# Kernel tuning notes

Hardware: AMD Instinct MI355X
Metric: run time of the kernel (lower is better)

Reference implementation:

```python
import jax, jax.numpy as jnp
import numpy as np
from jax import lax

B, L, D_MODEL = 8, 2048, 512
D_STATE, D_CONV, EXPAND = 16, 4, 2
D_INNER = EXPAND * D_MODEL          # 1024
DT_RANK = (D_MODEL + 15) // 16      # 32


def setup_inputs() -> dict:
    key = jax.random.key(0)
    ks = jax.random.split(key, 12)
    g = lambda k, shape, s=0.02: jax.random.normal(k, shape, jnp.float32) * s
    inp = {
        "p_history": jax.random.normal(ks[0], (B, L, D_MODEL), jnp.float32),
        "W_in":   g(ks[1], (2 * D_INNER, D_MODEL)),
        "conv_w": g(ks[2], (D_INNER, D_CONV), 0.1),
        "conv_b": jnp.zeros((D_INNER,), jnp.float32),
        "W_x":    g(ks[3], (DT_RANK + 2 * D_STATE, D_INNER)),
        "W_dt":   g(ks[4], (D_INNER, DT_RANK), 0.1),
        "b_dt":   g(ks[5], (D_INNER,), 0.5),
        "A_log":  jnp.log(jnp.broadcast_to(jnp.arange(1, D_STATE + 1, dtype=jnp.float32), (D_INNER, D_STATE))),
        "D":      jnp.ones((D_INNER,), jnp.float32),
        "W_out":  g(ks[6], (D_MODEL, D_INNER)),
        "ln_g":   jnp.ones((D_MODEL,), jnp.float32),
        "ln_b":   jnp.zeros((D_MODEL,), jnp.float32),
        "W_head": g(ks[7], (D_MODEL, D_MODEL)),
        "b_head": jnp.zeros((D_MODEL,), jnp.float32),
    }
    return inp


def _mamba_forward(p_history, W_in, conv_w, conv_b, W_x, W_dt, b_dt, A_log, D, W_out):
    # input projection -> x (ssm branch) and z (gate branch), each [B, L, d_inner]
    xz = jnp.einsum("bld,ed->ble", p_history, W_in)
    x, z = jnp.split(xz, 2, axis=-1)

    # depthwise causal conv over L: [B, d_inner, L]
    xc = x.swapaxes(1, 2)
    xc = lax.conv_general_dilated(
        xc, conv_w[:, None, :], window_strides=(1,),
        padding=[(D_CONV - 1, 0)], feature_group_count=D_INNER,
        dimension_numbers=("NCH", "OIH", "NCH"))
    xc = xc + conv_b[None, :, None]
    x = jax.nn.silu(xc.swapaxes(1, 2))  # [B, L, d_inner]

    # input-dependent dt, B, C
    x_dbl = jnp.einsum("blf,ef->ble", x, W_x)
    dt, Bm, Cm = jnp.split(x_dbl, [DT_RANK, DT_RANK + D_STATE], axis=-1)
    dt = jax.nn.softplus(jnp.einsum("blr,er->ble", dt, W_dt) + b_dt)  # [B, L, d_inner]

    A = -jnp.exp(A_log)  # [d_inner, d_state]

    def step(h, inp):
        dt_t, B_t, C_t, x_t = inp                   # [B,d_inner],[B,d_state],[B,d_state],[B,d_inner]
        dA = jnp.exp(dt_t[..., None] * A)           # [B, d_inner, d_state]
        h = dA * h + dt_t[..., None] * B_t[:, None, :] * x_t[..., None]
        y = jnp.einsum("bds,bs->bd", h, C_t)
        return h, y

    h0 = jnp.zeros((B, D_INNER, D_STATE), x.dtype)
    _, ys = lax.scan(step, h0, (dt.swapaxes(0, 1), Bm.swapaxes(0, 1),
                                Cm.swapaxes(0, 1), x.swapaxes(0, 1)))
    y = ys.swapaxes(0, 1) + x * D                   # skip connection
    y = y * jax.nn.silu(z)
    return jnp.einsum("ble,de->bld", y, W_out)      # [B, L, d_model]


def reference(p_history, W_in, conv_w, conv_b, W_x, W_dt, b_dt, A_log, D, W_out,
              ln_g, ln_b, W_head, b_head):
    out = _mamba_forward(p_history, W_in, conv_w, conv_b, W_x, W_dt, b_dt, A_log, D, W_out)
    mu = out.mean(-1, keepdims=True)
    var = ((out - mu) ** 2).mean(-1, keepdims=True)
    xn = (out - mu) * lax.rsqrt(var + 1e-5) * ln_g + ln_b
    return jnp.einsum("bd,ed->be", xn[:, -1, :], W_head) + b_head  # [B, d_model]
```

## Files before the change

### kernel.cpp

```cpp
#include <hip/hip_runtime.h>


#define NB 8
#define SEQ 2048
#define DM 512
#define DI 1024
#define DS 16
#define DR 32
#define NTOK (NB*SEQ)
#define NCH 64
#define CHL (SEQ/NCH)

typedef __attribute__((ext_vector_type(8))) short short8;
typedef __attribute__((ext_vector_type(4))) float f32x4;

__device__ __forceinline__ float b2f(unsigned short u){
  union { unsigned int i; float f; } v; v.i = ((unsigned int)u) << 16; return v.f;
}
__device__ __forceinline__ unsigned short f2b(float f){
  union { unsigned int i; float f; } v; v.f = f;
  unsigned int r = (v.i + 0x7FFFu + ((v.i >> 16) & 1u)) >> 16;
  return (unsigned short)r;
}
__device__ __forceinline__ float silu_(float x){ return x / (1.f + __expf(-x)); }
__device__ __forceinline__ float softplus_(float x){
  return fmaxf(x, 0.f) + __logf(1.f + __expf(-fabsf(x)));
}

typedef __attribute__((address_space(1))) const unsigned int g_u32;
typedef __attribute__((address_space(3))) unsigned int l_u32;
__device__ __forceinline__ void gl16(const void* g, void* l){
  __builtin_amdgcn_global_load_lds((g_u32*)g, (l_u32*)l, 16, 0, 0);
}

__global__ __launch_bounds__(256) void k_cvt(const float* __restrict__ src,
                                             unsigned short* __restrict__ dst, int n4){
  int i = blockIdx.x * 256 + threadIdx.x;
  if (i < n4){
    float4 v = reinterpret_cast<const float4*>(src)[i];
    ushort4 o;
    o.x = f2b(v.x); o.y = f2b(v.y); o.z = f2b(v.z); o.w = f2b(v.w);
    reinterpret_cast<ushort4*>(dst)[i] = o;
  }
}

__global__ __launch_bounds__(256) void k_cvt3(const float* __restrict__ s0, const float* __restrict__ s1,
                                              const float* __restrict__ s2,
                                              unsigned short* __restrict__ d0_, unsigned short* __restrict__ d1_,
                                              unsigned short* __restrict__ d2_){
  int i = blockIdx.x * 256 + threadIdx.x;
  const float* s; unsigned short* d; int j;
  if (i < 131072){ s = s0; d = d0_; j = i; }
  else if (i < 147456){ s = s1; d = d1_; j = i - 131072; }
  else { s = s2; d = d2_; j = i - 147456; }
  float4 v = reinterpret_cast<const float4*>(s)[j];
  ushort4 o; o.x = f2b(v.x); o.y = f2b(v.y); o.z = f2b(v.z); o.w = f2b(v.w);
  reinterpret_cast<ushort4*>(d)[j] = o;
}

__global__ __launch_bounds__(256) void k_gemm_x(const unsigned short* __restrict__ Ag,
                                                const unsigned short* __restrict__ Bg,
                                                unsigned short* __restrict__ xraw){
  __shared__ __align__(16) unsigned short smA[128*64];
  __shared__ __align__(16) unsigned short smB[128*64];
  int tid  = threadIdx.x;
  int lane = tid & 63, wv = tid >> 6;
  int wr = wv >> 1, wc = wv & 1;
  int m0 = blockIdx.x * 128;
  int n0 = blockIdx.y * 128;
  int r16 = lane & 15, kg = lane >> 4;
  f32x4 acc[4][4];
  #pragma unroll
  for (int i = 0; i < 4; ++i)
    #pragma unroll
    for (int j = 0; j < 4; ++j) acc[i][j] = (f32x4){0.f,0.f,0.f,0.f};

  for (int kt = 0; kt < 8; ++kt){
    int k0 = kt * 64;
    #pragma unroll
    for (int r = 0; r < 4; ++r){
      int seg = r * 4 + wv;
      int row = seg * 8 + (lane >> 3);
      int c16 = (lane & 7) ^ (row & 7);
      gl16(Ag + (size_t)(m0 + row) * DM + k0 + c16 * 8, smA + seg * 512);
      gl16(Bg + (size_t)(n0 + row) * DM + k0 + c16 * 8, smB + seg * 512);
    }
    asm volatile("s_waitcnt vmcnt(0)" ::: "memory");
    __syncthreads();
    #pragma unroll
    for (int kk = 0; kk < 2; ++kk){
      short8 af[4], bf[4];
      #pragma unroll
      for (int mt = 0; mt < 4; ++mt){
        int row = wr * 64 + mt * 16 + r16;
        int c16 = ((kk << 2) | kg) ^ (row & 7);
        af[mt] = *reinterpret_cast<const short8*>(smA + row * 64 + c16 * 8);
      }
      #pragma unroll
      for (int nt = 0; nt < 4; ++nt){
        int row = wc * 64 + nt * 16 + r16;
        int c16 = ((kk << 2) | kg) ^ (row & 7);
        bf[nt] = *reinterpret_cast<const short8*>(smB + row * 64 + c16 * 8);
      }
      #pragma unroll
      for (int mt = 0; mt < 4; ++mt)
        #pragma unroll
        for (int nt = 0; nt < 4; ++nt)
          acc[mt][nt] = __builtin_amdgcn_mfma_f32_16x16x32_bf16(af[mt], bf[nt], acc[mt][nt], 0, 0, 0);
    }
    __syncthreads();
  }
  #pragma unroll
  for (int mt = 0; mt < 4; ++mt){
    int rbase = m0 + wr * 64 + mt * 16 + kg * 4;
    #pragma unroll
    for (int nt = 0; nt < 4; ++nt){
      int col = n0 + wc * 64 + nt * 16 + r16;
      #pragma unroll
      for (int r = 0; r < 4; ++r)
        xraw[(size_t)(rbase + r) * DI + col] = f2b(acc[mt][nt][r]);
    }
  }
}

__global__ __launch_bounds__(256) void k_conv(const unsigned short* __restrict__ xraw,
                                              const float* __restrict__ cw,
                                              const float* __restrict__ cb,
                                              unsigned short* __restrict__ xc){
  int tid = threadIdx.x;
  int e4  = tid << 2;
  int t0  = blockIdx.x * 16;
  int l0  = t0 & (SEQ - 1);
  float4 cw0 = reinterpret_cast<const float4*>(cw)[e4 + 0];
  float4 cw1 = reinterpret_cast<const float4*>(cw)[e4 + 1];
  float4 cw2 = reinterpret_cast<const float4*>(cw)[e4 + 2];
  float4 cw3 = reinterpret_cast<const float4*>(cw)[e4 + 3];
  float4 cb4 = *reinterpret_cast<const float4*>(cb + e4);
  float4 wm3, wm2, wm1;
  if (l0 == 0){
    wm3 = wm2 = wm1 = (float4){0.f, 0.f, 0.f, 0.f};
  } else {
    ushort4 a = *reinterpret_cast<const ushort4*>(xraw + (size_t)(t0 - 3) * DI + e4);
    ushort4 b = *reinterpret_cast<const ushort4*>(xraw + (size_t)(t0 - 2) * DI + e4);
    ushort4 c = *reinterpret_cast<const ushort4*>(xraw + (size_t)(t0 - 1) * DI + e4);
    wm3 = (float4){b2f(a.x), b2f(a.y), b2f(a.z), b2f(a.w)};
    wm2 = (float4){b2f(b.x), b2f(b.y), b2f(b.z), b2f(b.w)};
    wm1 = (float4){b2f(c.x), b2f(c.y), b2f(c.z), b2f(c.w)};
  }
  #pragma unroll 4
  for (int t = t0; t < t0 + 16; ++t){
    ushort4 xv = *reinterpret_cast<const ushort4*>(xraw + (size_t)t * DI + e4);
    float4 xf = (float4){b2f(xv.x), b2f(xv.y), b2f(xv.z), b2f(xv.w)};
    float a0 = cb4.x + cw0.x*wm3.x + cw0.y*wm2.x + cw0.z*wm1.x + cw0.w*xf.x;
    float a1 = cb4.y + cw1.x*wm3.y + cw1.y*wm2.y + cw1.z*wm1.y + cw1.w*xf.y;
    float a2 = cb4.z + cw2.x*wm3.z + cw2.y*wm2.z + cw2.z*wm1.z + cw2.w*xf.z;
    float a3 = cb4.w + cw3.x*wm3.w + cw3.y*wm2.w + cw3.z*wm1.w + cw3.w*xf.w;
    ushort4 o;
    o.x = f2b(silu_(a0)); o.y = f2b(silu_(a1)); o.z = f2b(silu_(a2)); o.w = f2b(silu_(a3));
    *reinterpret_cast<ushort4*>(xc + (size_t)t * DI + e4) = o;
    wm3 = wm2; wm2 = wm1; wm1 = xf;
  }
}

__global__ __launch_bounds__(256) void k_bfx(const unsigned short* __restrict__ Wxb,
                                             unsigned short* __restrict__ Bfx){
  int i = blockIdx.x * 256 + threadIdx.x;
  int lane = i & 63, nt = (i >> 6) & 3, kk = (i >> 8) & 1, s = i >> 9;
  short8 v = *reinterpret_cast<const short8*>(
      Wxb + (size_t)(nt * 16 + (lane & 15)) * DI + s * 64 + kk * 32 + (lane >> 4) * 8);
  *reinterpret_cast<short8*>(Bfx + (size_t)i * 8) = v;
}

__global__ __launch_bounds__(256) void k_gemm_xdbl(const unsigned short* __restrict__ xc,
                                                   const unsigned short* __restrict__ Bfx,
                                                   float* __restrict__ xpart){
  __shared__ __align__(16) unsigned short smA[64*64];
  int tid  = threadIdx.x;
  int lane = tid & 63, wv = tid >> 6;
  int m0 = blockIdx.x * 64;
  int ks = blockIdx.y;
  int r16 = lane & 15, kg = lane >> 4;
  f32x4 acc[4];
  #pragma unroll
  for (int i = 0; i < 4; ++i) acc[i] = (f32x4){0.f,0.f,0.f,0.f};
  for (int kt = 0; kt < 8; ++kt){
    int k0 = ks * 512 + kt * 64;
    #pragma unroll
    for (int r = 0; r < 2; ++r){
      int seg = r * 4 + wv;
      int row = seg * 8 + (lane >> 3);
      int c16 = (lane & 7) ^ (row & 7);
      gl16(xc + (size_t)(m0 + row) * DI + k0 + c16 * 8, smA + seg * 512);
    }
    asm volatile("s_waitcnt vmcnt(0)" ::: "memory");
    __syncthreads();
    int sglob = ks * 8 + kt;
    #pragma unroll
    for (int kk = 0; kk < 2; ++kk){
      int row = wv * 16 + r16;
      int c16 = ((kk << 2) | kg) ^ (row & 7);
      short8 af = *reinterpret_cast<const short8*>(smA + row * 64 + c16 * 8);
      #pragma unroll
      for (int nt = 0; nt < 4; ++nt){
        short8 bf = *reinterpret_cast<const short8*>(
            Bfx + ((((size_t)sglob * 2 + kk) * 4 + nt) * 64 + lane) * 8);
        acc[nt] = __builtin_amdgcn_mfma_f32_16x16x32_bf16(af, bf, acc[nt], 0, 0, 0);
      }
    }
    __syncthreads();
  }
  float* xp = xpart + (size_t)ks * NTOK * 64;
  int rbase = m0 + wv * 16 + kg * 4;
  #pragma unroll
  for (int nt = 0; nt < 4; ++nt){
    int col = nt * 16 + r16;
    #pragma unroll
    for (int r = 0; r < 4; ++r)
      xp[(size_t)(rbase + r) * 64 + col] = acc[nt][r];
  }
}

__global__ __launch_bounds__(256) void k_xdbl_fin(const float* __restrict__ xp0,
                                                  const float* __restrict__ xp1,
                                                  float* __restrict__ xdbl,
                                                  unsigned short* __restrict__ dtraw){
  int i = blockIdx.x * 256 + threadIdx.x;
  float4 a = reinterpret_cast<const float4*>(xp0)[i];
  float4 b = reinterpret_cast<const float4*>(xp1)[i];
  float4 s = (float4){a.x + b.x, a.y + b.y, a.z + b.z, a.w + b.w};
  reinterpret_cast<float4*>(xdbl)[i] = s;
  int c4 = i & 15;
  if (c4 < 8){
    int row = i >> 4;
    ushort4 o;
    o.x = f2b(s.x); o.y = f2b(s.y); o.z = f2b(s.z); o.w = f2b(s.w);
    *reinterpret_cast<ushort4*>(dtraw + (size_t)row * DR + c4 * 4) = o;
  }
}

__global__ __launch_bounds__(256) void k_dt(const unsigned short* __restrict__ dtraw,
                                            const unsigned short* __restrict__ Wdtb,
                                            const float* __restrict__ bdt,
                                            unsigned short* __restrict__ dtb){
  int lane = threadIdx.x & 63;
  int wv   = threadIdx.x >> 6;
  int m0 = blockIdx.x * 64 + wv * 16;
  int r16 = lane & 15;
  int kg  = lane >> 4;
  short8 a = *reinterpret_cast<const short8*>(dtraw + (size_t)(m0 + r16) * DR + kg * 8);
  #pragma unroll
  for (int nt = 0; nt < 4; ++nt){
    int n0 = blockIdx.y * 64 + nt * 16;
    short8 b = *reinterpret_cast<const short8*>(Wdtb + (size_t)(n0 + r16) * DR + kg * 8);
    f32x4 acc = {0.f, 0.f, 0.f, 0.f};
    acc = __builtin_amdgcn_mfma_f32_16x16x32_bf16(a, b, acc, 0, 0, 0);
    int rbase = m0 + kg * 4;
    int col = n0 + r16;
    float bb = bdt[col];
    #pragma unroll
    for (int r = 0; r < 4; ++r)
      dtb[(size_t)(rbase + r) * DI + col] = f2b(softplus_(acc[r] + bb));
  }
}

__global__ __launch_bounds__(256) void k_zlast(const float* __restrict__ P,
                                               const float* __restrict__ Win,
                                               float* __restrict__ zl){
  __shared__ float sP[DM];
  int b = blockIdx.y, tid = threadIdx.x;
  const float* pr = P + ((size_t)b * SEQ + (SEQ - 1)) * DM;
  if (tid < 128) reinterpret_cast<float4*>(sP)[tid] = reinterpret_cast<const float4*>(pr)[tid];
  __syncthreads();
  int e  = blockIdx.x * 32 + (tid >> 3);
  int kc = tid & 7;
  const float4* wr = reinterpret_cast<const float4*>(Win + (size_t)(DI + e) * DM + kc * 64);
  const float4* pv = reinterpret_cast<const float4*>(sP + kc * 64);
  float acc = 0.f;
  #pragma unroll
  for (int i = 0; i < 16; ++i){
    float4 w4 = wr[i], p4 = pv[i];
    acc += w4.x*p4.x + w4.y*p4.y + w4.z*p4.z + w4.w*p4.w;
  }
  acc += __shfl_down(acc, 4, 8);
  acc += __shfl_down(acc, 2, 8);
  acc += __shfl_down(acc, 1, 8);
  if (kc == 0) zl[b * DI + e] = acc;
}

__global__ __launch_bounds__(256) void k_scan(const unsigned short* __restrict__ dtb,
                                              const unsigned short* __restrict__ xc,
                                              const float* __restrict__ xdbl,
                                              unsigned short* __restrict__ hcb,
                                              float* __restrict__ Sdt){
  __shared__ float sB[CHL*16];
  int tid = threadIdx.x;
  int d0 = blockIdx.x << 8;
  int c  = blockIdx.y;
  int b  = blockIdx.z;
  size_t tok0 = (size_t)b * SEQ + (size_t)c * CHL;
  if (tid < CHL * 4){
    int t = tid >> 2, j = tid & 3;
    *reinterpret_cast<float4*>(&sB[t * 16 + j * 4]) =
        *reinterpret_cast<const float4*>(xdbl + (tok0 + t) * 64 + DR + j * 4);
  }
  __syncthreads();
  int d = d0 + tid;
  const unsigned short* pdt = dtb + tok0 * DI + d;
  const unsigned short* px  = xc  + tok0 * DI + d;
  f32x4 h0 = {0,0,0,0}, h1 = {0,0,0,0}, h2 = {0,0,0,0}, h3 = {0,0,0,0};
  float S = 0.f;
  #pragma unroll 4
  for (int t = 0; t < CHL; ++t){
    float dtv = b2f(pdt[(size_t)t * DI]);
    float xv  = b2f(px[(size_t)t * DI]);
    float u = dtv * xv;
    S += dtv;
    float q = __expf(-dtv);
    float q2 = q * q, q3 = q2 * q, q4 = q2 * q2;
    f32x4 p0 = {q, q2, q3, q4};
    f32x4 q4v = {q4, q4, q4, q4};
    f32x4 p1 = p0 * q4v, p2 = p1 * q4v, p3 = p2 * q4v;
    const f32x4* B4 = reinterpret_cast<const f32x4*>(&sB[t * 16]);
    f32x4 uv = {u, u, u, u};
    h0 = p0 * h0 + uv * B4[0];
    h1 = p1 * h1 + uv * B4[1];
    h2 = p2 * h2 + uv * B4[2];
    h3 = p3 * h3 + uv * B4[3];
  }
  size_t o = (((size_t)(b * NCH + c) * DI + d) << 4);
  ushort4 o0, o1, o2, o3;
  o0.x = f2b(h0[0]); o0.y = f2b(h0[1]); o0.z = f2b(h0[2]); o0.w = f2b(h0[3]);
  o1.x = f2b(h1[0]); o1.y = f2b(h1[1]); o1.z = f2b(h1[2]); o1.w = f2b(h1[3]);
  o2.x = f2b(h2[0]); o2.y = f2b(h2[1]); o2.z = f2b(h2[2]); o2.w = f2b(h2[3]);
  o3.x = f2b(h3[0]); o3.y = f2b(h3[1]); o3.z = f2b(h3[2]); o3.w = f2b(h3[3]);
  ushort4* ph = reinterpret_cast<ushort4*>(hcb + o);
  ph[0] = o0; ph[1] = o1; ph[2] = o2; ph[3] = o3;
  Sdt[((size_t)(b * NCH + c) * DI) + d] = S;
}

__global__ __launch_bounds__(256) void k_combine(const unsigned short* __restrict__ hcb,
                                                 const float* __restrict__ Sdt,
                                                 const float* __restrict__ xdbl,
                                                 const unsigned short* __restrict__ xc,
                                                 const float* __restrict__ Dp,
                                                 const float* __restrict__ zl,
                                                 float* __restrict__ yg){
  int idx = blockIdx.x * 256 + threadIdx.x;
  int s = idx & 15;
  int d = (idx >> 4) & (DI - 1);
  int b = idx >> 14;
  float sp1 = -(float)(s + 1);
  float H = 0.f;
  #pragma unroll 8
  for (int c = 0; c < NCH; ++c){
    size_t base = ((size_t)(b * NCH + c) * DI + d);
    float P = __expf(sp1 * Sdt[base]);
    float hc = b2f(hcb[(base << 4) + s]);
    H = P * H + hc;
  }
  float C = xdbl[((size_t)b * SEQ + SEQ - 1) * 64 + 48 + s];
  float y = H * C;
  y += __shfl_xor(y, 1, 16);
  y += __shfl_xor(y, 2, 16);
  y += __shfl_xor(y, 4, 16);
  y += __shfl_xor(y, 8, 16);
  if (s == 0){
    float xl = b2f(xc[((size_t)b * SEQ + SEQ - 1) * DI + d]);
    float z  = zl[b * DI + d];
    yg[b * DI + d] = (y + xl * Dp[d]) * silu_(z);
  }
}

__global__ __launch_bounds__(256) void k_out(const float* __restrict__ yg,
                                             const float* __restrict__ Wout,
                                             float* __restrict__ outl){
  __shared__ float sY[DI];
  int b = blockIdx.y, tid = threadIdx.x;
  reinterpret_cast<float4*>(sY)[tid] = reinterpret_cast<const float4*>(yg + (size_t)b * DI)[tid];
  __syncthreads();
  int m  = blockIdx.x * 32 + (tid >> 3);
  int kc = tid & 7;
  const float4* wr = reinterpret_cast<const float4*>(Wout + (size_t)m * DI + kc * 128);
  const float4* yv = reinterpret_cast<const float4*>(sY + kc * 128);
  float acc = 0.f;
  #pragma unroll
  for (int i = 0; i < 32; ++i){
    float4 w4 = wr[i], y4 = yv[i];
    acc += w4.x*y4.x + w4.y*y4.y + w4.z*y4.z + w4.w*y4.w;
  }
  acc += __shfl_down(acc, 4, 8);
  acc += __shfl_down(acc, 2, 8);
  acc += __shfl_down(acc, 1, 8);
  if (kc == 0) outl[b * DM + m] = acc;
}

__global__ __launch_bounds__(256) void k_head(const float* __restrict__ outl,
                                              const float* __restrict__ lng,
                                              const float* __restrict__ lnb,
                                              const float* __restrict__ Wh,
                                              const float* __restrict__ bh,
                                              float* __restrict__ dout){
  __shared__ float red[256];
  __shared__ float sxn[DM];
  int b = blockIdx.y, tid = threadIdx.x;
  float v0 = outl[b * DM + tid];
  float v1 = outl[b * DM + tid + 256];
  red[tid] = v0 + v1;
  __syncthreads();
  for (int st = 128; st > 0; st >>= 1){
    if (tid < st) red[tid] += red[tid + st];
    __syncthreads();
  }
  float mu = red[0] * (1.f / DM);
  __syncthreads();
  float a0 = v0 - mu, a1 = v1 - mu;
  red[tid] = a0*a0 + a1*a1;
  __syncthreads();
  for (int st = 128; st > 0; st >>= 1){
    if (tid < st) red[tid] += red[tid + st];
    __syncthreads();
  }
  float rs = rsqrtf(red[0] * (1.f / DM) + 1e-5f);
  sxn[tid]       = a0 * rs * lng[tid]       + lnb[tid];
  sxn[tid + 256] = a1 * rs * lng[tid + 256] + lnb[tid + 256];
  __syncthreads();
  int e  = blockIdx.x * 32 + (tid >> 3);
  int kc = tid & 7;
  const float4* wr = reinterpret_cast<const float4*>(Wh + (size_t)e * DM + kc * 64);
  const float4* xv = reinterpret_cast<const float4*>(sxn + kc * 64);
  float acc = 0.f;
  #pragma unroll
  for (int i = 0; i < 16; ++i){
    float4 w4 = wr[i], x4 = xv[i];
    acc += w4.x*x4.x + w4.y*x4.y + w4.z*x4.z + w4.w*x4.w;
  }
  acc += __shfl_down(acc, 4, 8);
  acc += __shfl_down(acc, 2, 8);
  acc += __shfl_down(acc, 1, 8);
  if (kc == 0) dout[b * DM + e] = acc + bh[e];
}

extern "C" void kernel_launch(void* const* d_in, const int* in_sizes, int n_in,
                              void* d_out, int out_size, void* d_ws, size_t ws_size,
                              hipStream_t stream) {
  const float* P    = (const float*)d_in[0];
  const float* Win  = (const float*)d_in[1];
  const float* cw   = (const float*)d_in[2];
  const float* cb   = (const float*)d_in[3];
  const float* Wx   = (const float*)d_in[4];
  const float* Wdt  = (const float*)d_in[5];
  const float* bdt  = (const float*)d_in[6];
  const float* Dp   = (const float*)d_in[8];
  const float* Wout = (const float*)d_in[9];
  const float* lng  = (const float*)d_in[10];
  const float* lnb  = (const float*)d_in[11];
  const float* Wh   = (const float*)d_in[12];
  const float* bh   = (const float*)d_in[13];
  float* out = (float*)d_out;

  char* w = (char*)d_ws;
  unsigned short* Pb    = (unsigned short*)(w + 0);
  float*          xpart = (float*)(w + 0);
  unsigned short* Bfx   = (unsigned short*)(w + 8388608);
  unsigned short* hcb   = (unsigned short*)(w + 0);
  unsigned short* Wb    = (unsigned short*)(w + 16777216);
  unsigned short* Wxb   = (unsigned short*)(w + 17825792);
  unsigned short* Wdtb  = (unsigned short*)(w + 17956864);
  unsigned short* xraw  = (unsigned short*)(w + 18022400);
  unsigned short* xconv = (unsigned short*)(w + 51576832);
  float*          xdbl  = (float*)(w + 85131264);
  unsigned short* dtraw = (unsigned short*)(w + 89325568);
  float*          Sdt   = (float*)(w + 90374144);
  float*          zl    = (float*)(w + 107151360);
  float*          yg    = (float*)(w + 107184128);
  float*          outl  = (float*)(w + 107216896);
  unsigned short* dtb   = xraw;

  k_cvt<<<8192, 256, 0, stream>>>(P, Pb, (NTOK*DM)/4);
  k_cvt3<<<608, 256, 0, stream>>>(Win, Wx, Wdt, Wb, Wxb, Wdtb);
  k_zlast<<<dim3(32, NB), 256, 0, stream>>>(P, Win, zl);
  k_gemm_x<<<dim3(NTOK/128, DI/128), 256, 0, stream>>>(Pb, Wb, xraw);
  k_bfx<<<32, 256, 0, stream>>>(Wxb, Bfx);
  k_conv<<<NTOK/16, 256, 0, stream>>>(xraw, cw, cb, xconv);
  k_gemm_xdbl<<<dim3(NTOK/64, 2), 256, 0, stream>>>(xconv, Bfx, xpart);
  k_xdbl_fin<<<1024, 256, 0, stream>>>(xpart, xpart + (size_t)NTOK*64, xdbl, dtraw);
  k_dt<<<dim3(NTOK/64, DI/64), 256, 0, stream>>>(dtraw, Wdtb, bdt, dtb);
  k_scan<<<dim3(DI/256, NCH, NB), 256, 0, stream>>>(dtb, xconv, xdbl, hcb, Sdt);
  k_combine<<<(NB*DI*DS)/256, 256, 0, stream>>>(hcb, Sdt, xdbl, xconv, Dp, zl, yg);
  k_out<<<dim3(16, NB), 256, 0, stream>>>(yg, Wout, outl);
  k_head<<<dim3(16, NB), 256, 0, stream>>>(outl, lng, lnb, Wh, bh, out);
}
```

Baseline: 138.3 us.

## Fuse fp32-to-bf16 conversion of activations into input GEMM and remap tiles

Drops the separate pass that converted p_history to bf16. The input-projection GEMM now loads fp32 rows into registers, converts them, and writes them to swizzled LDS, prefetching the next k-tile's fp32 data during compute. Blocks are remapped so that consecutive blocks share the same A rows across the 8 N tiles, which should improve L2 reuse. W_x conversion moves into k_bfx. This removes a 32MB fp32 read and a 16MB bf16 round trip, but the GEMM now reads fp32 A (twice the bytes) and carries more register pressure.

```diff
diff --git a/kernel.cpp b/kernel.cpp
--- a/kernel.cpp
+++ b/kernel.cpp
@@ -33,32 +33,18 @@
   __builtin_amdgcn_global_load_lds((g_u32*)g, (l_u32*)l, 16, 0, 0);
 }
 
-__global__ __launch_bounds__(256) void k_cvt(const float* __restrict__ src,
-                                             unsigned short* __restrict__ dst, int n4){
-  int i = blockIdx.x * 256 + threadIdx.x;
-  if (i < n4){
-    float4 v = reinterpret_cast<const float4*>(src)[i];
-    ushort4 o;
-    o.x = f2b(v.x); o.y = f2b(v.y); o.z = f2b(v.z); o.w = f2b(v.w);
-    reinterpret_cast<ushort4*>(dst)[i] = o;
-  }
-}
-
-__global__ __launch_bounds__(256) void k_cvt3(const float* __restrict__ s0, const float* __restrict__ s1,
-                                              const float* __restrict__ s2,
-                                              unsigned short* __restrict__ d0_, unsigned short* __restrict__ d1_,
-                                              unsigned short* __restrict__ d2_){
+__global__ __launch_bounds__(256) void k_cvt2(const float* __restrict__ s0, const float* __restrict__ s1,
+                                              unsigned short* __restrict__ d0_, unsigned short* __restrict__ d1_){
   int i = blockIdx.x * 256 + threadIdx.x;
   const float* s; unsigned short* d; int j;
   if (i < 131072){ s = s0; d = d0_; j = i; }
-  else if (i < 147456){ s = s1; d = d1_; j = i - 131072; }
-  else { s = s2; d = d2_; j = i - 147456; }
+  else { s = s1; d = d1_; j = i - 131072; }
   float4 v = reinterpret_cast<const float4*>(s)[j];
   ushort4 o; o.x = f2b(v.x); o.y = f2b(v.y); o.z = f2b(v.z); o.w = f2b(v.w);
   reinterpret_cast<ushort4*>(d)[j] = o;
 }
 
-__global__ __launch_bounds__(256) void k_gemm_x(const unsigned short* __restrict__ Ag,
+__global__ __launch_bounds__(256) void k_gemm_x(const float* __restrict__ Ag,
                                                 const unsigned short* __restrict__ Bg,
                                                 unsigned short* __restrict__ xraw){
   __shared__ __align__(16) unsigned short smA[128*64];
@@ -66,8 +52,10 @@
   int tid  = threadIdx.x;
   int lane = tid & 63, wv = tid >> 6;
   int wr = wv >> 1, wc = wv & 1;
-  int m0 = blockIdx.x * 128;
-  int n0 = blockIdx.y * 128;
+  int lin  = blockIdx.x;
+  int virt = (lin & 7) * 128 + (lin >> 3);
+  int m0 = (virt >> 3) * 128;
+  int n0 = (virt & 7) * 128;
   int r16 = lane & 15, kg = lane >> 4;
   f32x4 acc[4][4];
   #pragma unroll
@@ -75,18 +63,48 @@
     #pragma unroll
     for (int j = 0; j < 4; ++j) acc[i][j] = (f32x4){0.f,0.f,0.f,0.f};
 
+  float4 aLo[4], aHi[4];
+  #pragma unroll
+  for (int r = 0; r < 4; ++r){
+    int idx = r * 256 + tid;
+    int row = idx >> 3, g = idx & 7;
+    const float4* src = reinterpret_cast<const float4*>(Ag + (size_t)(m0 + row) * DM + g * 8);
+    aLo[r] = src[0]; aHi[r] = src[1];
+  }
+
   for (int kt = 0; kt < 8; ++kt){
     int k0 = kt * 64;
+    #pragma unroll
+    for (int r = 0; r < 4; ++r){
+      int idx = r * 256 + tid;
+      int row = idx >> 3, g = idx & 7;
+      int gs = g ^ (row & 7);
+      short8 v;
+      v[0] = (short)f2b(aLo[r].x); v[1] = (short)f2b(aLo[r].y);
+      v[2] = (short)f2b(aLo[r].z); v[3] = (short)f2b(aLo[r].w);
+      v[4] = (short)f2b(aHi[r].x); v[5] = (short)f2b(aHi[r].y);
+      v[6] = (short)f2b(aHi[r].z); v[7] = (short)f2b(aHi[r].w);
+      *reinterpret_cast<short8*>(smA + row * 64 + gs * 8) = v;
+    }
     #pragma unroll
     for (int r = 0; r < 4; ++r){
       int seg = r * 4 + wv;
       int row = seg * 8 + (lane >> 3);
       int c16 = (lane & 7) ^ (row & 7);
-      gl16(Ag + (size_t)(m0 + row) * DM + k0 + c16 * 8, smA + seg * 512);
       gl16(Bg + (size_t)(n0 + row) * DM + k0 + c16 * 8, smB + seg * 512);
     }
     asm volatile("s_waitcnt vmcnt(0)" ::: "memory");
     __syncthreads();
+    if (kt < 7){
+      int k1 = k0 + 64;
+      #pragma unroll
+      for (int r = 0; r < 4; ++r){
+        int idx = r * 256 + tid;
+        int row = idx >> 3, g = idx & 7;
+        const float4* src = reinterpret_cast<const float4*>(Ag + (size_t)(m0 + row) * DM + k1 + g * 8);
+        aLo[r] = src[0]; aHi[r] = src[1];
+      }
+    }
     #pragma unroll
     for (int kk = 0; kk < 2; ++kk){
       short8 af[4], bf[4];
@@ -162,12 +180,16 @@
   }
 }
 
-__global__ __launch_bounds__(256) void k_bfx(const unsigned short* __restrict__ Wxb,
+__global__ __launch_bounds__(256) void k_bfx(const float* __restrict__ Wx,
                                              unsigned short* __restrict__ Bfx){
   int i = blockIdx.x * 256 + threadIdx.x;
   int lane = i & 63, nt = (i >> 6) & 3, kk = (i >> 8) & 1, s = i >> 9;
-  short8 v = *reinterpret_cast<const short8*>(
-      Wxb + (size_t)(nt * 16 + (lane & 15)) * DI + s * 64 + kk * 32 + (lane >> 4) * 8);
+  const float4* src = reinterpret_cast<const float4*>(
+      Wx + (size_t)(nt * 16 + (lane & 15)) * DI + s * 64 + kk * 32 + (lane >> 4) * 8);
+  float4 lo = src[0], hi = src[1];
+  short8 v;
+  v[0] = (short)f2b(lo.x); v[1] = (short)f2b(lo.y); v[2] = (short)f2b(lo.z); v[3] = (short)f2b(lo.w);
+  v[4] = (short)f2b(hi.x); v[5] = (short)f2b(hi.y); v[6] = (short)f2b(hi.z); v[7] = (short)f2b(hi.w);
   *reinterpret_cast<short8*>(Bfx + (size_t)i * 8) = v;
 }
 
@@ -459,12 +481,10 @@
   float* out = (float*)d_out;
 
   char* w = (char*)d_ws;
-  unsigned short* Pb    = (unsigned short*)(w + 0);
   float*          xpart = (float*)(w + 0);
   unsigned short* Bfx   = (unsigned short*)(w + 8388608);
   unsigned short* hcb   = (unsigned short*)(w + 0);
   unsigned short* Wb    = (unsigned short*)(w + 16777216);
-  unsigned short* Wxb   = (unsigned short*)(w + 17825792);
   unsigned short* Wdtb  = (unsigned short*)(w + 17956864);
   unsigned short* xraw  = (unsigned short*)(w + 18022400);
   unsigned short* xconv = (unsigned short*)(w + 51576832);
@@ -476,11 +496,10 @@
   float*          outl  = (float*)(w + 107216896);
   unsigned short* dtb   = xraw;
 
-  k_cvt<<<8192, 256, 0, stream>>>(P, Pb, (NTOK*DM)/4);
-  k_cvt3<<<608, 256, 0, stream>>>(Win, Wx, Wdt, Wb, Wxb, Wdtb);
+  k_cvt2<<<544, 256, 0, stream>>>(Win, Wdt, Wb, Wdtb);
   k_zlast<<<dim3(32, NB), 256, 0, stream>>>(P, Win, zl);
-  k_gemm_x<<<dim3(NTOK/128, DI/128), 256, 0, stream>>>(Pb, Wb, xraw);
-  k_bfx<<<32, 256, 0, stream>>>(Wxb, Bfx);
+  k_gemm_x<<<1024, 256, 0, stream>>>(P, Wb, xraw);
+  k_bfx<<<32, 256, 0, stream>>>(Wx, Bfx);
   k_conv<<<NTOK/16, 256, 0, stream>>>(xraw, cw, cb, xconv);
   k_gemm_xdbl<<<dim3(NTOK/64, 2), 256, 0, stream>>>(xconv, Bfx, xpart);
   k_xdbl_fin<<<1024, 256, 0, stream>>>(xpart, xpart + (size_t)NTOK*64, xdbl, dtraw);
```

After: 137.7 us. No clear change (-0.4%).
